# Kernel optimization log

Measured on AMD Instinct MI355X. Metric: run time of the kernel, lower is better.

Reference implementation:

```python
import jax, jax.numpy as jnp
import numpy as np

N = 100000      # total nodes (batched graphs)
E = 1200000     # total edges
A = 256         # annotation size (hidden_size_orig)
H = 64          # gnn_h_size
T = 4           # num_edge_types
STEPS = 6       # num_timesteps
B = 64          # number of graphs in the batch
NUM_CLS = 2


def setup_inputs() -> dict:
    key = jax.random.key(0)
    ks = jax.random.split(key, 16)
    annotation = jax.random.normal(ks[0], (N, A), dtype=jnp.float32)
    src = jax.random.randint(ks[1], (E,), 0, N, dtype=jnp.int32)
    dst = jax.random.randint(ks[2], (E,), 0, N, dtype=jnp.int32)
    etypes = jax.random.randint(ks[3], (E,), 0, T, dtype=jnp.int32)
    graph_ids = jnp.sort(jax.random.randint(ks[4], (N,), 0, B, dtype=jnp.int32))

    def lin(k, fan_in, shape):
        return jax.random.normal(k, shape, dtype=jnp.float32) / np.sqrt(fan_in).astype(np.float32)

    params = {
        'reduce_W': lin(ks[5], A, (A, H)),
        'reduce_b': jnp.zeros((H,), jnp.float32),
        'edge_W': lin(ks[6], H, (T, H, H)),      # per-edge-type linear
        'edge_b': jnp.zeros((T, H), jnp.float32),
        'gru_Wi': lin(ks[7], H, (3 * H, H)),     # torch GRUCell layout: r,z,n
        'gru_bi': jnp.zeros((3 * H,), jnp.float32),
        'gru_Wh': lin(ks[8], H, (3 * H, H)),
        'gru_bh': jnp.zeros((3 * H,), jnp.float32),
        'gate_W': lin(ks[9], 2 * H, (2 * H, 1)),
        'gate_b': jnp.zeros((1,), jnp.float32),
        'out_W': lin(ks[10], 2 * H, (2 * H, NUM_CLS)),
        'out_b': jnp.zeros((NUM_CLS,), jnp.float32),
    }
    return dict(annotation=annotation, src=src, dst=dst, etypes=etypes,
                graph_ids=graph_ids, **params)


def reference(annotation, src, dst, etypes, graph_ids,
              reduce_W, reduce_b, edge_W, edge_b,
              gru_Wi, gru_bi, gru_Wh, gru_bh,
              gate_W, gate_b, out_W, out_b):
    # reduce_layer
    h0 = annotation @ reduce_W + reduce_b            # [N, H]

    def step(h, _):
        # per-edge-type linear on all nodes: [T, N, H]
        transformed = jnp.einsum('nh,thk->tnk', h, edge_W) + edge_b[:, None, :]
        msg = transformed[etypes, src]               # [E, H] gather per edge
        a = jax.ops.segment_sum(msg, dst, num_segments=N)  # scatter-add
        # GRUCell(a, h)
        gi = a @ gru_Wi.T + gru_bi
        gh = h @ gru_Wh.T + gru_bh
        i_r, i_z, i_n = jnp.split(gi, 3, axis=-1)
        h_r, h_z, h_n = jnp.split(gh, 3, axis=-1)
        r = jax.nn.sigmoid(i_r + h_r)
        z = jax.nn.sigmoid(i_z + h_z)
        n = jnp.tanh(i_n + r * h_n)
        h_new = (1.0 - z) * n + z * h
        return h_new, None

    h, _ = jax.lax.scan(step, h0, None, length=STEPS)

    feat = jnp.concatenate([h, h0], axis=-1)         # [N, 2H]

    # GlobalAttentionPooling: segment softmax over gate scores, weighted sum
    gate = feat @ gate_W + gate_b                    # [N, 1]
    gmax = jax.ops.segment_max(gate, graph_ids, num_segments=B)
    gmax = jnp.where(jnp.isfinite(gmax), gmax, 0.0)  # guard empty graphs
    e = jnp.exp(gate - gmax[graph_ids])
    denom = jax.ops.segment_sum(e, graph_ids, num_segments=B)
    alpha = e / denom[graph_ids]                     # [N, 1]
    readout = jax.ops.segment_sum(alpha * feat, graph_ids, num_segments=B)  # [B, 2H]

    logits = readout @ out_W + out_b                 # [B, 2]
    return logits
```

## Files before the change

kernel.cpp:

```cpp
#include <hip/hip_runtime.h>
#include <cstdint>
#include <cstddef>

#define N_NODES 100000
#define N_EDGES 1200000
#define ASIZE 256
#define HSIZE 64
#define NTYPES 4
#define NSTEPS 6
#define NGRAPH 64

static __device__ __forceinline__ float sigmoidf_(float x) { return 1.0f / (1.0f + expf(-x)); }

__global__ void k_count(const int* __restrict__ dst, int* __restrict__ deg) {
    int e = blockIdx.x * 256 + threadIdx.x;
    if (e < N_EDGES) atomicAdd(&deg[dst[e]], 1);
}

__global__ void k_scan1(const int* __restrict__ deg, int* __restrict__ rs, int* __restrict__ part) {
    __shared__ int sh[256];
    int t = threadIdx.x;
    int base = blockIdx.x * 1024 + t * 4;
    int v0 = (base + 0 < N_NODES) ? deg[base + 0] : 0;
    int v1 = (base + 1 < N_NODES) ? deg[base + 1] : 0;
    int v2 = (base + 2 < N_NODES) ? deg[base + 2] : 0;
    int v3 = (base + 3 < N_NODES) ? deg[base + 3] : 0;
    int s = v0 + v1 + v2 + v3;
    sh[t] = s;
    __syncthreads();
    for (int off = 1; off < 256; off <<= 1) {
        int x = (t >= off) ? sh[t - off] : 0;
        __syncthreads();
        sh[t] += x;
        __syncthreads();
    }
    int excl = sh[t] - s;
    if (t == 255) part[blockIdx.x] = sh[255];
    if (base + 0 < N_NODES) rs[base + 0] = excl;
    if (base + 1 < N_NODES) rs[base + 1] = excl + v0;
    if (base + 2 < N_NODES) rs[base + 2] = excl + v0 + v1;
    if (base + 3 < N_NODES) rs[base + 3] = excl + v0 + v1 + v2;
}

__global__ void k_scan2(int* __restrict__ part, int* __restrict__ rs, int nb) {
    if (threadIdx.x == 0 && blockIdx.x == 0) {
        int run = 0;
        for (int i = 0; i < nb; ++i) { int v = part[i]; part[i] = run; run += v; }
        rs[N_NODES] = run;
    }
}

__global__ void k_scan3(int* __restrict__ rs, const int* __restrict__ part) {
    int i = blockIdx.x * 256 + threadIdx.x;
    if (i < N_NODES) rs[i] += part[i >> 10];
}

__global__ void k_fill(const int* __restrict__ src, const int* __restrict__ dst,
                       const int* __restrict__ ety, const int* __restrict__ rs,
                       int* __restrict__ cur, int* __restrict__ colidx) {
    int e = blockIdx.x * 256 + threadIdx.x;
    if (e < N_EDGES) {
        int d = dst[e];
        int pos = rs[d] + atomicAdd(&cur[d], 1);
        colidx[pos] = src[e] * 448 + 192 + ety[e] * 64;
    }
}

__global__ void k_prep2(const float* __restrict__ Wh, const float* __restrict__ Bh,
                        const float* __restrict__ eW, const float* __restrict__ eb,
                        const float* __restrict__ Wi, const float* __restrict__ Bi,
                        float* __restrict__ W448, float* __restrict__ bias448,
                        float* __restrict__ WiA, float* __restrict__ biA) {
    int idx = blockIdx.x * 256 + threadIdx.x;
    if (idx < 64 * 448) {
        int k = idx / 448, m = idx % 448;
        float v;
        if (m < 192) {
            int j = m / 3, g = m % 3;
            v = Wh[(g * 64 + j) * 64 + k];
        } else {
            v = eW[(size_t)(m - 192 >> 6) * 4096 + k * 64 + ((m - 192) & 63)];
        }
        W448[idx] = v;
    }
    if (idx < 64 * 192) {
        int k = idx / 192, m = idx % 192;
        int j = m / 3, g = m % 3;
        WiA[idx] = Wi[(g * 64 + j) * 64 + k];
    }
    if (idx < 448) {
        bias448[idx] = (idx < 192) ? Bh[(idx % 3) * 64 + idx / 3] : eb[idx - 192];
    }
    if (idx < 192) {
        biA[idx] = Bi[(idx % 3) * 64 + idx / 3];
    }
}

__global__ __launch_bounds__(256) void k_gemm(const float* __restrict__ X, int ldx, int K,
                                              const float* __restrict__ W, int ldw,
                                              const float* __restrict__ bias,
                                              float* __restrict__ Y, float* __restrict__ Y2,
                                              int M) {
    __shared__ float sX[128 * 66];
    __shared__ float sW[64 * 64];
    int tid = threadIdx.x;
    int mtile = blockIdx.x * 64;
    int ntile = blockIdx.y * 128;
    int tc4 = (tid & 15) * 4;
    int tr = tid >> 4;
    float4 acc[8];
#pragma unroll
    for (int i = 0; i < 8; ++i) acc[i] = make_float4(0.f, 0.f, 0.f, 0.f);

    int nkc = K >> 6;
    for (int kc = 0; kc < nkc; ++kc) {
        if (kc) __syncthreads();
#pragma unroll
        for (int i = 0; i < 8; ++i) {
            int lin4 = (i * 256 + tid) * 4;
            int nl = lin4 >> 6, kk = lin4 & 63;
            int n = ntile + nl;
            float4 v = make_float4(0.f, 0.f, 0.f, 0.f);
            if (n < N_NODES) v = *(const float4*)(X + (size_t)n * ldx + kc * 64 + kk);
            float* d = sX + nl * 66 + kk;
            d[0] = v.x; d[1] = v.y; d[2] = v.z; d[3] = v.w;
        }
#pragma unroll
        for (int i = 0; i < 4; ++i) {
            int lin4 = (i * 256 + tid) * 4;
            int kk = lin4 >> 6, c = lin4 & 63;
            float4 v = *(const float4*)(W + (size_t)(kc * 64 + kk) * ldw + mtile + c);
            *(float4*)(sW + kk * 64 + c) = v;
        }
        __syncthreads();
        const float* xr = sX + tr * 8 * 66;
        const float* wr = sW + tc4;
        for (int kk = 0; kk < 64; kk += 2) {
            float4 wA = *(const float4*)(wr + kk * 64);
            float4 wB = *(const float4*)(wr + (kk + 1) * 64);
            float xA[8], xB[8];
#pragma unroll
            for (int i = 0; i < 8; ++i) { xA[i] = xr[i * 66 + kk]; xB[i] = xr[i * 66 + kk + 1]; }
#pragma unroll
            for (int i = 0; i < 8; ++i) {
                acc[i].x = fmaf(xA[i], wA.x, acc[i].x);
                acc[i].y = fmaf(xA[i], wA.y, acc[i].y);
                acc[i].z = fmaf(xA[i], wA.z, acc[i].z);
                acc[i].w = fmaf(xA[i], wA.w, acc[i].w);
            }
#pragma unroll
            for (int i = 0; i < 8; ++i) {
                acc[i].x = fmaf(xB[i], wB.x, acc[i].x);
                acc[i].y = fmaf(xB[i], wB.y, acc[i].y);
                acc[i].z = fmaf(xB[i], wB.z, acc[i].z);
                acc[i].w = fmaf(xB[i], wB.w, acc[i].w);
            }
        }
    }
    float4 bv = *(const float4*)(bias + mtile + tc4);
#pragma unroll
    for (int i = 0; i < 8; ++i) {
        int n = ntile + tr * 8 + i;
        if (n < N_NODES) {
            float4 y;
            y.x = acc[i].x + bv.x; y.y = acc[i].y + bv.y;
            y.z = acc[i].z + bv.z; y.w = acc[i].w + bv.w;
            *(float4*)(Y + (size_t)n * M + mtile + tc4) = y;
            if (Y2) *(float4*)(Y2 + (size_t)n * M + mtile + tc4) = y;
        }
    }
}

__global__ void k_aggregate(const float* __restrict__ buf1, const int* __restrict__ rs,
                            const int* __restrict__ colidx, float* __restrict__ a) {
    int l = threadIdx.x & 63;
    int n = blockIdx.x * 4 + (threadIdx.x >> 6);
    int beg = rs[n], end = rs[n + 1];
    float acc0 = 0.f, acc1 = 0.f;
    int s = beg;
    for (; s + 1 < end; s += 2) {
        int c0 = colidx[s], c1 = colidx[s + 1];
        acc0 += buf1[(size_t)c0 + l];
        acc1 += buf1[(size_t)c1 + l];
    }
    if (s < end) acc0 += buf1[(size_t)colidx[s] + l];
    a[(size_t)n * 64 + l] = acc0 + acc1;
}

__global__ __launch_bounds__(256) void k_gruF(const float* __restrict__ A,
                                              const float* __restrict__ WiA,
                                              const float* __restrict__ biA,
                                              const float* __restrict__ buf1,
                                              float* __restrict__ H) {
    __shared__ float sX[64 * 34];
    __shared__ float sW[32 * 192];
    int tid = threadIdx.x;
    int ntile = blockIdx.x * 64;
    int tc = tid & 15;
    int tr = tid >> 4;
    float acc[4][12];
#pragma unroll
    for (int i = 0; i < 4; ++i)
#pragma unroll
        for (int c = 0; c < 12; ++c) acc[i][c] = 0.f;

    for (int kc = 0; kc < 2; ++kc) {
        if (kc) __syncthreads();
#pragma unroll
        for (int i = 0; i < 2; ++i) {
            int lin4 = (i * 256 + tid) * 4;
            int nl = lin4 >> 5, kk = lin4 & 31;
            int n = ntile + nl;
            float4 v = make_float4(0.f, 0.f, 0.f, 0.f);
            if (n < N_NODES) v = *(const float4*)(A + (size_t)n * 64 + kc * 32 + kk);
            float* d = sX + nl * 34 + kk;
            d[0] = v.x; d[1] = v.y; d[2] = v.z; d[3] = v.w;
        }
        {
            int kk = tid >> 3, c = (tid & 7) * 24;
            const float* srcp = WiA + (size_t)(kc * 32 + kk) * 192 + c;
            float* d = sW + kk * 192 + c;
#pragma unroll
            for (int u = 0; u < 6; ++u) *(float4*)(d + 4 * u) = *(const float4*)(srcp + 4 * u);
        }
        __syncthreads();
        const float* xr = sX + tr * 4 * 34;
        const float* wr = sW + tc * 12;
        for (int kk = 0; kk < 32; kk += 2) {
            float4 w0 = *(const float4*)(wr + kk * 192);
            float4 w1 = *(const float4*)(wr + kk * 192 + 4);
            float4 w2 = *(const float4*)(wr + kk * 192 + 8);
            float4 u0 = *(const float4*)(wr + (kk + 1) * 192);
            float4 u1 = *(const float4*)(wr + (kk + 1) * 192 + 4);
            float4 u2 = *(const float4*)(wr + (kk + 1) * 192 + 8);
            float xA[4], xB[4];
#pragma unroll
            for (int i = 0; i < 4; ++i) { xA[i] = xr[i * 34 + kk]; xB[i] = xr[i * 34 + kk + 1]; }
#pragma unroll
            for (int i = 0; i < 4; ++i) {
                acc[i][0]  = fmaf(xA[i], w0.x, acc[i][0]);
                acc[i][1]  = fmaf(xA[i], w0.y, acc[i][1]);
                acc[i][2]  = fmaf(xA[i], w0.z, acc[i][2]);
                acc[i][3]  = fmaf(xA[i], w0.w, acc[i][3]);
                acc[i][4]  = fmaf(xA[i], w1.x, acc[i][4]);
                acc[i][5]  = fmaf(xA[i], w1.y, acc[i][5]);
                acc[i][6]  = fmaf(xA[i], w1.z, acc[i][6]);
                acc[i][7]  = fmaf(xA[i], w1.w, acc[i][7]);
                acc[i][8]  = fmaf(xA[i], w2.x, acc[i][8]);
                acc[i][9]  = fmaf(xA[i], w2.y, acc[i][9]);
                acc[i][10] = fmaf(xA[i], w2.z, acc[i][10]);
                acc[i][11] = fmaf(xA[i], w2.w, acc[i][11]);
            }
#pragma unroll
            for (int i = 0; i < 4; ++i) {
                acc[i][0]  = fmaf(xB[i], u0.x, acc[i][0]);
                acc[i][1]  = fmaf(xB[i], u0.y, acc[i][1]);
                acc[i][2]  = fmaf(xB[i], u0.z, acc[i][2]);
                acc[i][3]  = fmaf(xB[i], u0.w, acc[i][3]);
                acc[i][4]  = fmaf(xB[i], u1.x, acc[i][4]);
                acc[i][5]  = fmaf(xB[i], u1.y, acc[i][5]);
                acc[i][6]  = fmaf(xB[i], u1.z, acc[i][6]);
                acc[i][7]  = fmaf(xB[i], u1.w, acc[i][7]);
                acc[i][8]  = fmaf(xB[i], u2.x, acc[i][8]);
                acc[i][9]  = fmaf(xB[i], u2.y, acc[i][9]);
                acc[i][10] = fmaf(xB[i], u2.z, acc[i][10]);
                acc[i][11] = fmaf(xB[i], u2.w, acc[i][11]);
            }
        }
    }
    float bb[12];
    {
        float4 b0 = *(const float4*)(biA + tc * 12);
        float4 b1 = *(const float4*)(biA + tc * 12 + 4);
        float4 b2 = *(const float4*)(biA + tc * 12 + 8);
        bb[0] = b0.x; bb[1] = b0.y; bb[2] = b0.z; bb[3] = b0.w;
        bb[4] = b1.x; bb[5] = b1.y; bb[6] = b1.z; bb[7] = b1.w;
        bb[8] = b2.x; bb[9] = b2.y; bb[10] = b2.z; bb[11] = b2.w;
    }
#pragma unroll
    for (int i = 0; i < 4; ++i) {
        int n = ntile + tr * 4 + i;
        if (n >= N_NODES) continue;
        const float* ghp = buf1 + (size_t)n * 448 + tc * 12;
        float gg[12];
        float4 g0 = *(const float4*)(ghp);
        float4 g1 = *(const float4*)(ghp + 4);
        float4 g2 = *(const float4*)(ghp + 8);
        gg[0] = g0.x; gg[1] = g0.y; gg[2] = g0.z; gg[3] = g0.w;
        gg[4] = g1.x; gg[5] = g1.y; gg[6] = g1.z; gg[7] = g1.w;
        gg[8] = g2.x; gg[9] = g2.y; gg[10] = g2.z; gg[11] = g2.w;
        float4 hv = *(const float4*)(H + (size_t)n * 64 + tc * 4);
        float res[4];
#pragma unroll
        for (int jj = 0; jj < 4; ++jj) {
            int c = jj * 3;
            float r = sigmoidf_(acc[i][c] + bb[c] + gg[c]);
            float z = sigmoidf_(acc[i][c + 1] + bb[c + 1] + gg[c + 1]);
            float nn = tanhf(acc[i][c + 2] + bb[c + 2] + r * gg[c + 2]);
            float hj = (jj == 0) ? hv.x : (jj == 1) ? hv.y : (jj == 2) ? hv.z : hv.w;
            res[jj] = (1.f - z) * nn + z * hj;
        }
        float4 o; o.x = res[0]; o.y = res[1]; o.z = res[2]; o.w = res[3];
        *(float4*)(H + (size_t)n * 64 + tc * 4) = o;
    }
}

__global__ void k_bounds(const int* __restrict__ gid, int* __restrict__ start) {
    int n = blockIdx.x * 256 + threadIdx.x;
    if (n < N_NODES) {
        int g = gid[n];
        if (n == 0) {
            for (int x = 0; x <= g; ++x) start[x] = 0;
        } else {
            int pg = gid[n - 1];
            for (int x = pg + 1; x <= g; ++x) start[x] = n;
        }
        if (n == N_NODES - 1) {
            for (int x = g + 1; x <= NGRAPH; ++x) start[x] = N_NODES;
        }
    }
}

__global__ void k_gate2(const float* __restrict__ H, const float* __restrict__ H0,
                        const float* __restrict__ gW, const float* __restrict__ gb,
                        float* __restrict__ gate) {
    int l = threadIdx.x & 63;
    int n = blockIdx.x * 4 + (threadIdx.x >> 6);
    float v = H[(size_t)n * 64 + l] * gW[l] + H0[(size_t)n * 64 + l] * gW[64 + l];
    for (int off = 32; off > 0; off >>= 1) v += __shfl_xor(v, off, 64);
    if (l == 0) gate[n] = v + gb[0];
}

__global__ __launch_bounds__(256) void k_pool(const float* __restrict__ H,
                                              const float* __restrict__ H0,
                                              const float* __restrict__ gate,
                                              const int* __restrict__ start,
                                              float* __restrict__ ro) {
    int g = blockIdx.x;
    int beg = start[g], end = start[g + 1];
    int t = threadIdx.x;
    int lane = t & 63, wave = t >> 6;
    __shared__ float sred[256];
    __shared__ float shh[4][64], sh0[4][64];

    float m = -INFINITY;
    for (int n = beg + t; n < end; n += 256) m = fmaxf(m, gate[n]);
    sred[t] = m; __syncthreads();
    for (int off = 128; off > 0; off >>= 1) {
        if (t < off) sred[t] = fmaxf(sred[t], sred[t + off]);
        __syncthreads();
    }
    m = sred[0];
    if (!isfinite(m)) m = 0.0f;
    __syncthreads();

    float s = 0.f;
    for (int n = beg + t; n < end; n += 256) s += expf(gate[n] - m);
    sred[t] = s; __syncthreads();
    for (int off = 128; off > 0; off >>= 1) {
        if (t < off) sred[t] += sred[t + off];
        __syncthreads();
    }
    float inv_denom = 1.0f / sred[0];
    __syncthreads();

    float ah = 0.f, ah0 = 0.f;
    for (int n = beg + wave; n < end; n += 4) {
        float alpha = expf(gate[n] - m) * inv_denom;
        ah  += alpha * H [(size_t)n * 64 + lane];
        ah0 += alpha * H0[(size_t)n * 64 + lane];
    }
    shh[wave][lane] = ah; sh0[wave][lane] = ah0;
    __syncthreads();
    if (wave == 0) {
        float r  = shh[0][lane] + shh[1][lane] + shh[2][lane] + shh[3][lane];
        float r0 = sh0[0][lane] + sh0[1][lane] + sh0[2][lane] + sh0[3][lane];
        ro[g * 128 + lane]      = r;
        ro[g * 128 + 64 + lane] = r0;
    }
}

__global__ void k_logits(const float* __restrict__ ro, const float* __restrict__ oW,
                         const float* __restrict__ ob, float* __restrict__ out) {
    int t = threadIdx.x;
    int b = t >> 1;
    int c = t & 1;
    float acc = ob[c];
    for (int k = 0; k < 128; ++k) acc = fmaf(ro[b * 128 + k], oW[k * 2 + c], acc);
    out[b * 2 + c] = acc;
}

extern "C" void kernel_launch(void* const* d_in, const int* in_sizes, int n_in,
                              void* d_out, int out_size, void* d_ws, size_t ws_size,
                              hipStream_t stream) {
    (void)in_sizes; (void)n_in; (void)out_size; (void)ws_size;
    const float* ann = (const float*)d_in[0];
    const int* src   = (const int*)d_in[1];
    const int* dst   = (const int*)d_in[2];
    const int* ety   = (const int*)d_in[3];
    const int* gid   = (const int*)d_in[4];
    const float* rW  = (const float*)d_in[5];
    const float* rb  = (const float*)d_in[6];
    const float* eW  = (const float*)d_in[7];
    const float* eb  = (const float*)d_in[8];
    const float* Wi  = (const float*)d_in[9];
    const float* Bi  = (const float*)d_in[10];
    const float* Wh  = (const float*)d_in[11];
    const float* Bh  = (const float*)d_in[12];
    const float* gW  = (const float*)d_in[13];
    const float* gb  = (const float*)d_in[14];
    const float* oW  = (const float*)d_in[15];
    const float* ob  = (const float*)d_in[16];
    float* out = (float*)d_out;

    char* p = (char*)d_ws;
    auto take = [&](size_t nbytes) -> void* {
        void* r = (void*)p;
        p += (nbytes + 255) & ~((size_t)255);
        return r;
    };
    float* h0      = (float*)take((size_t)N_NODES * 64 * 4);
    float* h       = (float*)take((size_t)N_NODES * 64 * 4);
    float* abuf    = (float*)take((size_t)N_NODES * 64 * 4);
    float* buf1    = (float*)take((size_t)N_NODES * 448 * 4);
    float* W448    = (float*)take(64 * 448 * 4);
    float* bias448 = (float*)take(448 * 4);
    float* WiA     = (float*)take(64 * 192 * 4);
    float* biA     = (float*)take(192 * 4);
    int* deg       = (int*)take((size_t)N_NODES * 4);
    int* cur       = (int*)take((size_t)N_NODES * 4);
    int* rs        = (int*)take((size_t)(N_NODES + 1) * 4);
    int* part      = (int*)take(512);
    int* colidx    = (int*)take((size_t)N_EDGES * 4);
    float* gate    = (float*)take((size_t)N_NODES * 4);
    int* start     = (int*)take((size_t)(NGRAPH + 1) * 4);
    float* ro      = (float*)take(NGRAPH * 128 * 4);

    hipMemsetAsync(deg, 0, (size_t)N_NODES * 4, stream);
    hipMemsetAsync(cur, 0, (size_t)N_NODES * 4, stream);
    k_count<<<(N_EDGES + 255) / 256, 256, 0, stream>>>(dst, deg);
    int nb = (N_NODES + 1023) / 1024;
    k_scan1<<<nb, 256, 0, stream>>>(deg, rs, part);
    k_scan2<<<1, 64, 0, stream>>>(part, rs, nb);
    k_scan3<<<(N_NODES + 255) / 256, 256, 0, stream>>>(rs, part);
    k_fill<<<(N_EDGES + 255) / 256, 256, 0, stream>>>(src, dst, ety, rs, cur, colidx);

    k_prep2<<<112, 256, 0, stream>>>(Wh, Bh, eW, eb, Wi, Bi, W448, bias448, WiA, biA);
    k_bounds<<<(N_NODES + 255) / 256, 256, 0, stream>>>(gid, start);

    int ntiles = (N_NODES + 127) / 128;

    k_gemm<<<dim3(1, ntiles), 256, 0, stream>>>(ann, ASIZE, ASIZE, rW, 64, rb, h, h0, 64);

    for (int s = 0; s < NSTEPS; ++s) {
        k_gemm<<<dim3(7, ntiles), 256, 0, stream>>>(h, 64, 64, W448, 448, bias448,
                                                    buf1, nullptr, 448);
        k_aggregate<<<N_NODES / 4, 256, 0, stream>>>(buf1, rs, colidx, abuf);
        k_gruF<<<(N_NODES + 63) / 64, 256, 0, stream>>>(abuf, WiA, biA, buf1, h);
    }

    k_gate2<<<N_NODES / 4, 256, 0, stream>>>(h, h0, gW, gb, gate);
    k_pool<<<NGRAPH, 256, 0, stream>>>(h, h0, gate, start, ro);
    k_logits<<<1, 128, 0, stream>>>(ro, oW, ob, out);
}
```

Measured before the change: 1.771 ms.

## Fuse edge aggregation into GRU kernel and split attention pooling across graph slices

The per-step gather/scatter aggregation is moved into the GRU kernel: each block builds its 64-node aggregated message tile directly in shared memory, which removes the abuf write/read round trip and one launch per step. The attention pooling, which used only 64 blocks, is split into four kernels that compute per-slice partial maxima, partial exp-sums and weighted feature sums over 16 slices per graph, then combine them. This gives the pooling far more parallelism at the cost of extra launches and small partial buffers. The fused GRU kernel now holds an irregular gather phase before its GEMM, which may hurt its latency hiding.

Result: slower. 2.293 ms (+29.5%).

```diff
diff --git a/kernel.cpp b/kernel.cpp
--- a/kernel.cpp
+++ b/kernel.cpp
@@ -9,6 +9,7 @@
 #define NTYPES 4
 #define NSTEPS 6
 #define NGRAPH 64
+#define PS 16
 
 static __device__ __forceinline__ float sigmoidf_(float x) { return 1.0f / (1.0f + expf(-x)); }
 
@@ -171,31 +172,36 @@
     }
 }
 
-__global__ void k_aggregate(const float* __restrict__ buf1, const int* __restrict__ rs,
-                            const int* __restrict__ colidx, float* __restrict__ a) {
-    int l = threadIdx.x & 63;
-    int n = blockIdx.x * 4 + (threadIdx.x >> 6);
-    int beg = rs[n], end = rs[n + 1];
-    float acc0 = 0.f, acc1 = 0.f;
-    int s = beg;
-    for (; s + 1 < end; s += 2) {
-        int c0 = colidx[s], c1 = colidx[s + 1];
-        acc0 += buf1[(size_t)c0 + l];
-        acc1 += buf1[(size_t)c1 + l];
-    }
-    if (s < end) acc0 += buf1[(size_t)colidx[s] + l];
-    a[(size_t)n * 64 + l] = acc0 + acc1;
-}
-
-__global__ __launch_bounds__(256) void k_gruF(const float* __restrict__ A,
+__global__ __launch_bounds__(256) void k_gruF(const float* __restrict__ buf1,
                                               const float* __restrict__ WiA,
                                               const float* __restrict__ biA,
-                                              const float* __restrict__ buf1,
+                                              const int* __restrict__ rs,
+                                              const int* __restrict__ colidx,
                                               float* __restrict__ H) {
-    __shared__ float sX[64 * 34];
+    __shared__ float sA[64 * 66];
     __shared__ float sW[32 * 192];
     int tid = threadIdx.x;
     int ntile = blockIdx.x * 64;
+    int wave = tid >> 6, lane = tid & 63;
+
+    for (int ii = 0; ii < 16; ++ii) {
+        int nl = wave * 16 + ii;
+        int n = ntile + nl;
+        float acc0 = 0.f, acc1 = 0.f;
+        if (n < N_NODES) {
+            int beg = rs[n], end = rs[n + 1];
+            int s = beg;
+            for (; s + 1 < end; s += 2) {
+                int c0 = colidx[s], c1 = colidx[s + 1];
+                acc0 += buf1[(size_t)c0 + lane];
+                acc1 += buf1[(size_t)c1 + lane];
+            }
+            if (s < end) acc0 += buf1[(size_t)colidx[s] + lane];
+        }
+        sA[nl * 66 + lane] = acc0 + acc1;
+    }
+    __syncthreads();
+
     int tc = tid & 15;
     int tr = tid >> 4;
     float acc[4][12];
@@ -206,16 +212,6 @@
 
     for (int kc = 0; kc < 2; ++kc) {
         if (kc) __syncthreads();
-#pragma unroll
-        for (int i = 0; i < 2; ++i) {
-            int lin4 = (i * 256 + tid) * 4;
-            int nl = lin4 >> 5, kk = lin4 & 31;
-            int n = ntile + nl;
-            float4 v = make_float4(0.f, 0.f, 0.f, 0.f);
-            if (n < N_NODES) v = *(const float4*)(A + (size_t)n * 64 + kc * 32 + kk);
-            float* d = sX + nl * 34 + kk;
-            d[0] = v.x; d[1] = v.y; d[2] = v.z; d[3] = v.w;
-        }
         {
             int kk = tid >> 3, c = (tid & 7) * 24;
             const float* srcp = WiA + (size_t)(kc * 32 + kk) * 192 + c;
@@ -224,7 +220,7 @@
             for (int u = 0; u < 6; ++u) *(float4*)(d + 4 * u) = *(const float4*)(srcp + 4 * u);
         }
         __syncthreads();
-        const float* xr = sX + tr * 4 * 34;
+        const float* xr = sA + tr * 4 * 66 + kc * 32;
         const float* wr = sW + tc * 12;
         for (int kk = 0; kk < 32; kk += 2) {
             float4 w0 = *(const float4*)(wr + kk * 192);
@@ -235,7 +231,7 @@
             float4 u2 = *(const float4*)(wr + (kk + 1) * 192 + 8);
             float xA[4], xB[4];
 #pragma unroll
-            for (int i = 0; i < 4; ++i) { xA[i] = xr[i * 34 + kk]; xB[i] = xr[i * 34 + kk + 1]; }
+            for (int i = 0; i < 4; ++i) { xA[i] = xr[i * 66 + kk]; xB[i] = xr[i * 66 + kk + 1]; }
 #pragma unroll
             for (int i = 0; i < 4; ++i) {
                 acc[i][0]  = fmaf(xA[i], w0.x, acc[i][0]);
@@ -331,53 +327,72 @@
     if (l == 0) gate[n] = v + gb[0];
 }
 
-__global__ __launch_bounds__(256) void k_pool(const float* __restrict__ H,
-                                              const float* __restrict__ H0,
-                                              const float* __restrict__ gate,
+__global__ __launch_bounds__(64) void k_poolA(const float* __restrict__ gate,
                                               const int* __restrict__ start,
-                                              float* __restrict__ ro) {
-    int g = blockIdx.x;
-    int beg = start[g], end = start[g + 1];
+                                              float* __restrict__ pmax) {
+    int g = blockIdx.x, s = blockIdx.y;
+    int beg = start[g], len = start[g + 1] - beg;
+    int sb = beg + (int)((long long)len * s / PS);
+    int se = beg + (int)((long long)len * (s + 1) / PS);
+    float m = -INFINITY;
+    for (int n = sb + threadIdx.x; n < se; n += 64) m = fmaxf(m, gate[n]);
+    for (int off = 32; off > 0; off >>= 1) m = fmaxf(m, __shfl_xor(m, off, 64));
+    if (threadIdx.x == 0) pmax[g * PS + s] = m;
+}
+
+__global__ void k_poolB(const float* __restrict__ pmax, float* __restrict__ gm) {
+    int g = threadIdx.x;
+    float m = -INFINITY;
+    for (int s = 0; s < PS; ++s) m = fmaxf(m, pmax[g * PS + s]);
+    if (!isfinite(m)) m = 0.0f;
+    gm[g] = m;
+}
+
+__global__ __launch_bounds__(256) void k_poolC(const float* __restrict__ H,
+                                               const float* __restrict__ H0,
+                                               const float* __restrict__ gate,
+                                               const int* __restrict__ start,
+                                               const float* __restrict__ gm,
+                                               float* __restrict__ pnum,
+                                               float* __restrict__ pden) {
+    int g = blockIdx.x, s = blockIdx.y;
+    int beg = start[g], len = start[g + 1] - beg;
+    int sb = beg + (int)((long long)len * s / PS);
+    int se = beg + (int)((long long)len * (s + 1) / PS);
     int t = threadIdx.x;
     int lane = t & 63, wave = t >> 6;
-    __shared__ float sred[256];
-    __shared__ float shh[4][64], sh0[4][64];
-
-    float m = -INFINITY;
-    for (int n = beg + t; n < end; n += 256) m = fmaxf(m, gate[n]);
-    sred[t] = m; __syncthreads();
-    for (int off = 128; off > 0; off >>= 1) {
-        if (t < off) sred[t] = fmaxf(sred[t], sred[t + off]);
-        __syncthreads();
-    }
-    m = sred[0];
-    if (!isfinite(m)) m = 0.0f;
-    __syncthreads();
-
-    float s = 0.f;
-    for (int n = beg + t; n < end; n += 256) s += expf(gate[n] - m);
-    sred[t] = s; __syncthreads();
-    for (int off = 128; off > 0; off >>= 1) {
-        if (t < off) sred[t] += sred[t + off];
-        __syncthreads();
-    }
-    float inv_denom = 1.0f / sred[0];
-    __syncthreads();
-
-    float ah = 0.f, ah0 = 0.f;
-    for (int n = beg + wave; n < end; n += 4) {
-        float alpha = expf(gate[n] - m) * inv_denom;
-        ah  += alpha * H [(size_t)n * 64 + lane];
-        ah0 += alpha * H0[(size_t)n * 64 + lane];
+    float m = gm[g];
+    __shared__ float shh[4][64], sh0[4][64], ses[4];
+    float ah = 0.f, ah0 = 0.f, es = 0.f;
+    for (int n = sb + wave; n < se; n += 4) {
+        float e = expf(gate[n] - m);
+        es += e;
+        ah  += e * H [(size_t)n * 64 + lane];
+        ah0 += e * H0[(size_t)n * 64 + lane];
     }
     shh[wave][lane] = ah; sh0[wave][lane] = ah0;
+    if (lane == 0) ses[wave] = es;
     __syncthreads();
     if (wave == 0) {
         float r  = shh[0][lane] + shh[1][lane] + shh[2][lane] + shh[3][lane];
         float r0 = sh0[0][lane] + sh0[1][lane] + sh0[2][lane] + sh0[3][lane];
-        ro[g * 128 + lane]      = r;
-        ro[g * 128 + 64 + lane] = r0;
-    }
+        int base = (g * PS + s) * 128;
+        pnum[base + lane]      = r;
+        pnum[base + 64 + lane] = r0;
+        if (lane == 0) pden[g * PS + s] = ses[0] + ses[1] + ses[2] + ses[3];
+    }
+}
+
+__global__ __launch_bounds__(128) void k_poolD(const float* __restrict__ pnum,
+                                               const float* __restrict__ pden,
+                                               float* __restrict__ ro) {
+    int g = blockIdx.x;
+    int c = threadIdx.x;
+    float den = 0.f;
+    for (int s = 0; s < PS; ++s) den += pden[g * PS + s];
+    float nu = 0.f;
+    for (int s = 0; s < PS; ++s) nu += pnum[(g * PS + s) * 128 + c];
+    ro[g * 128 + c] = (den > 0.f) ? nu / den : 0.f;
 }
 
 __global__ void k_logits(const float* __restrict__ ro, const float* __restrict__ oW,
@@ -421,7 +436,6 @@
     };
     float* h0      = (float*)take((size_t)N_NODES * 64 * 4);
     float* h       = (float*)take((size_t)N_NODES * 64 * 4);
-    float* abuf    = (float*)take((size_t)N_NODES * 64 * 4);
     float* buf1    = (float*)take((size_t)N_NODES * 448 * 4);
     float* W448    = (float*)take(64 * 448 * 4);
     float* bias448 = (float*)take(448 * 4);
@@ -434,6 +448,10 @@
     int* colidx    = (int*)take((size_t)N_EDGES * 4);
     float* gate    = (float*)take((size_t)N_NODES * 4);
     int* start     = (int*)take((size_t)(NGRAPH + 1) * 4);
+    float* pmax    = (float*)take(NGRAPH * PS * 4);
+    float* gm      = (float*)take(NGRAPH * 4);
+    float* pnum    = (float*)take((size_t)NGRAPH * PS * 128 * 4);
+    float* pden    = (float*)take(NGRAPH * PS * 4);
     float* ro      = (float*)take(NGRAPH * 128 * 4);
 
     hipMemsetAsync(deg, 0, (size_t)N_NODES * 4, stream);
@@ -455,11 +473,13 @@
     for (int s = 0; s < NSTEPS; ++s) {
         k_gemm<<<dim3(7, ntiles), 256, 0, stream>>>(h, 64, 64, W448, 448, bias448,
                                                     buf1, nullptr, 448);
-        k_aggregate<<<N_NODES / 4, 256, 0, stream>>>(buf1, rs, colidx, abuf);
-        k_gruF<<<(N_NODES + 63) / 64, 256, 0, stream>>>(abuf, WiA, biA, buf1, h);
+        k_gruF<<<(N_NODES + 63) / 64, 256, 0, stream>>>(buf1, WiA, biA, rs, colidx, h);
     }
 
     k_gate2<<<N_NODES / 4, 256, 0, stream>>>(h, h0, gW, gb, gate);
-    k_pool<<<NGRAPH, 256, 0, stream>>>(h, h0, gate, start, ro);
+    k_poolA<<<dim3(NGRAPH, PS), 64, 0, stream>>>(gate, start, pmax);
+    k_poolB<<<1, 64, 0, stream>>>(pmax, gm);
+    k_poolC<<<dim3(NGRAPH, PS), 256, 0, stream>>>(h, h0, gate, start, gm, pnum, pden);
+    k_poolD<<<NGRAPH, 128, 0, stream>>>(pnum, pden, ro);
     k_logits<<<1, 128, 0, stream>>>(ro, oW, ob, out);
 }
```
